# Kernel tuning notes

Measured on AMD Instinct MI355X. Metric: run time of the kernel, lower is better.

Reference implementation:

```python
import jax, jax.numpy as jnp
import numpy as np

B, S, D = 1, 4096, 1024
H, Dh = 16, 64
F = 4096  # mlp_factor * D
EPS = 1e-6


def _ln(x, scale, bias=None):
    m = jnp.mean(x, axis=-1, keepdims=True)
    v = jnp.var(x, axis=-1, keepdims=True)
    y = (x - m) * jax.lax.rsqrt(v + EPS) * scale
    return y + bias if bias is not None else y


def setup_inputs() -> dict:
    key = jax.random.key(0)
    ks = jax.random.split(key, 10)
    lecun = lambda k, shape, fan_in: (jax.random.normal(k, shape, jnp.float32) * (fan_in ** -0.5))
    inp = {
        "x": jax.random.normal(ks[0], (B, S, D), jnp.float32),
        # causal mask, broadcastable to [B, H, S, S]
        "mask": jnp.tril(jnp.ones((S, S), bool))[None, None],
        # PreNorm (TPNorm -> LayerNorm)
        "ln_scale": jnp.ones((D,), jnp.float32),
        "ln_bias": jnp.zeros((D,), jnp.float32),
        # MLP input projection
        "w_in": lecun(ks[1], (D, F), D),
        "b_in": jnp.zeros((F,), jnp.float32),
        # QKV projection
        "wq": lecun(ks[2], (D, H, Dh), D),
        "bq": jnp.zeros((H, Dh), jnp.float32),
        "wk": lecun(ks[3], (D, H, Dh), D),
        "bk": jnp.zeros((H, Dh), jnp.float32),
        "wv": lecun(ks[4], (D, H, Dh), D),
        "bv": jnp.zeros((H, Dh), jnp.float32),
        # qk-norm scales (normalize_qk=True)
        "qn_scale": jnp.ones((Dh,), jnp.float32),
        "kn_scale": jnp.ones((Dh,), jnp.float32),
        # MLP output projection
        "w_mo": lecun(ks[5], (F, D), F),
        "b_mo": jnp.zeros((D,), jnp.float32),
        # Attention output projection
        "w_ao": lecun(ks[6], (H * Dh, D), H * Dh),
        "b_ao": jnp.zeros((D,), jnp.float32),
    }
    return inp


def reference(x, mask, ln_scale, ln_bias, w_in, b_in, wq, bq, wk, bk, wv, bv,
              qn_scale, kn_scale, w_mo, b_mo, w_ao, b_ao):
    residual = x
    xn = _ln(x, ln_scale, ln_bias)

    # fused QKV + MLP-input projections (QKVMLPDenseParallel)
    h = jax.nn.gelu(jnp.einsum("bsd,df->bsf", xn, w_in) + b_in)  # [B,S,F]
    q = jnp.einsum("bsd,dhk->bshk", xn, wq) + bq  # [B,S,H,Dh]
    k = jnp.einsum("bsd,dhk->bshk", xn, wk) + bk
    v = jnp.einsum("bsd,dhk->bshk", xn, wv) + bv
    # normalize_qk: per-head LayerNorm (no bias) on q, k
    q = _ln(q, qn_scale)
    k = _ln(k, kn_scale)

    # dot-product attention
    scores = jnp.einsum("bqhd,bkhd->bhqk", q, k) / np.sqrt(Dh).astype(np.float32)
    scores = jnp.where(mask, scores, jnp.finfo(scores.dtype).min)
    attn = jax.nn.softmax(scores, axis=-1)
    o = jnp.einsum("bhqk,bkhd->bqhd", attn, v)  # [B,S,H,Dh]

    # fused attention-out + MLP-out projections (AttnMLPOutParallel)
    mlp_out = jnp.einsum("bsf,fd->bsd", h, w_mo) + b_mo
    attn_out = jnp.einsum("bse,ed->bsd", o.reshape(B, S, H * Dh), w_ao) + b_ao

    # dropout deterministic (train=False); residual add
    return residual + mlp_out + attn_out
```

## Files before the change

kernel.cpp:

```cpp
#include <hip/hip_runtime.h>
#include <hip/hip_fp16.h>

typedef _Float16 half8 __attribute__((ext_vector_type(8)));
typedef float floatx4 __attribute__((ext_vector_type(4)));

constexpr int kS = 4096;
constexpr int kD = 1024;
constexpr int kH = 16;
constexpr int kDh = 64;
constexpr int kF = 4096;
constexpr int kNQKV = kF + 3 * kD;
constexpr int kKOut = kF + kD;

__device__ __forceinline__ void async_ld16(const void* g, void* l) {
  __builtin_amdgcn_global_load_lds(
      (const __attribute__((address_space(1))) void*)g,
      (__attribute__((address_space(3))) void*)l, 16, 0, 0);
}

__global__ __launch_bounds__(256) void prep0_kernel(
    const float* __restrict__ w_in, const float* __restrict__ wq,
    const float* __restrict__ wk, const float* __restrict__ wv,
    const float* __restrict__ w_mo, const float* __restrict__ w_ao,
    _Float16* __restrict__ Wqkv, _Float16* __restrict__ Wout,
    const float* __restrict__ x, const float* __restrict__ ln_scale,
    const float* __restrict__ ln_bias, _Float16* __restrict__ xn) {
  __shared__ float t[32][33];
  __shared__ float red[8];
  int id = blockIdx.x;
  const int tid = threadIdx.x;

  if (id >= 12288) {
    const int row = id - 12288;
    const float* xr = x + (size_t)row * kD;
    float v[4];
    float s = 0.f, sq = 0.f;
#pragma unroll
    for (int i = 0; i < 4; ++i) {
      v[i] = xr[tid + 256 * i];
      s += v[i];
      sq += v[i] * v[i];
    }
    for (int off = 32; off; off >>= 1) {
      s += __shfl_xor(s, off);
      sq += __shfl_xor(sq, off);
    }
    const int wv2 = tid >> 6;
    if ((tid & 63) == 0) { red[wv2] = s; red[wv2 + 4] = sq; }
    __syncthreads();
    s = red[0] + red[1] + red[2] + red[3];
    sq = red[4] + red[5] + red[6] + red[7];
    const float mean = s * (1.0f / kD);
    const float var = sq * (1.0f / kD) - mean * mean;
    const float rstd = rsqrtf(var + 1e-6f);
#pragma unroll
    for (int i = 0; i < 4; ++i) {
      int d = tid + 256 * i;
      xn[(size_t)row * kD + d] = (_Float16)((v[i] - mean) * rstd * ln_scale[d] + ln_bias[d]);
    }
    return;
  }

  const float* src; _Float16* dst; int N, ldk, noff, koff, nt, kt;
  if (id < 4096)       { src = w_in; dst = Wqkv; N = kF; ldk = kD; noff = 0;        koff = 0;  nt = id & 127; kt = id >> 7; }
  else if (id < 5120)  { id -= 4096; src = wq;  dst = Wqkv; N = kD; ldk = kD; noff = kF;       koff = 0;  nt = id & 31; kt = id >> 5; }
  else if (id < 6144)  { id -= 5120; src = wk;  dst = Wqkv; N = kD; ldk = kD; noff = kF + kD;  koff = 0;  nt = id & 31; kt = id >> 5; }
  else if (id < 7168)  { id -= 6144; src = wv;  dst = Wqkv; N = kD; ldk = kD; noff = kF + 2*kD; koff = 0; nt = id & 31; kt = id >> 5; }
  else if (id < 11264) { id -= 7168; src = w_mo; dst = Wout; N = kD; ldk = kKOut; noff = 0;    koff = 0;  nt = id & 31; kt = id >> 5; }
  else                 { id -= 11264; src = w_ao; dst = Wout; N = kD; ldk = kKOut; noff = 0;   koff = kF; nt = id & 31; kt = id >> 5; }
  const int n0 = nt * 32, k0 = kt * 32;
#pragma unroll
  for (int i = 0; i < 4; ++i) {
    const int kl = (tid >> 5) + i * 8, nl = tid & 31;
    t[kl][nl] = src[(size_t)(k0 + kl) * N + n0 + nl];
  }
  __syncthreads();
#pragma unroll
  for (int i = 0; i < 4; ++i) {
    const int nl = (tid >> 5) + i * 8, kl = tid & 31;
    dst[(size_t)(noff + n0 + nl) * ldk + koff + k0 + kl] = (_Float16)t[kl][nl];
  }
}

__global__ __launch_bounds__(256) void htrans_kernel(
    const _Float16* __restrict__ src, _Float16* __restrict__ dst, int R, int C) {
  __shared__ _Float16 t[32][34];
  const int tid = threadIdx.x;
  const int c0 = blockIdx.x * 32, r0 = blockIdx.y * 32;
#pragma unroll
  for (int i = 0; i < 4; ++i) {
    const int rl = (tid >> 5) + i * 8, cl = tid & 31;
    t[rl][cl] = src[(size_t)(r0 + rl) * C + c0 + cl];
  }
  __syncthreads();
#pragma unroll
  for (int i = 0; i < 4; ++i) {
    const int cl = (tid >> 5) + i * 8, rl = tid & 31;
    dst[(size_t)(c0 + cl) * R + r0 + rl] = t[rl][cl];
  }
}

__device__ __forceinline__ float fast_gelu(float xv) {
  const float z = 0.7978845608028654f * (xv + 0.044715f * xv * xv * xv);
  const float u = exp2f(fminf(2.885390081777927f * z, 80.0f));
  return xv * u / (1.0f + u);
}

__global__ __launch_bounds__(256) void gemm_qkvin(
    const _Float16* __restrict__ A, const _Float16* __restrict__ Bp,
    const float* __restrict__ b_in, const float* __restrict__ bq,
    const float* __restrict__ bk, const float* __restrict__ bv,
    const float* __restrict__ qn_scale, const float* __restrict__ kn_scale,
    _Float16* __restrict__ ho, _Float16* __restrict__ q,
    _Float16* __restrict__ k, _Float16* __restrict__ v) {
  __shared__ alignas(16) _Float16 Ts[16 * 512];
  _Float16* As = Ts;
  _Float16* Bs = Ts + 8 * 512;

  const int tid = threadIdx.x;
  const int lane = tid & 63;
  const int wave = tid >> 6;
  const int wm = (wave >> 1) * 64;
  const int wn = (wave & 1) * 64;
  const int m0 = blockIdx.x * 128;
  const int n0 = blockIdx.y * 128;
  const int lrow = lane & 15;
  const int quad = lane >> 4;

  floatx4 acc[4][4] = {};

  for (int k0 = 0; k0 < kD; k0 += 32) {
    __syncthreads();
#pragma unroll
    for (int i = 0; i < 4; ++i) {
      const int chunk = wave * 4 + i;
      const int r = ((chunk & 7) << 4) + (lane >> 2);
      const int csrc = ((lane & 3) ^ ((r >> 1) & 3)) << 3;
      const _Float16* src = (chunk < 8)
          ? A + (size_t)(m0 + r) * kD + k0 + csrc
          : Bp + (size_t)(n0 + r) * kD + k0 + csrc;
      async_ld16(src, Ts + chunk * 512);
    }
    __syncthreads();

    half8 af[4], bf[4];
#pragma unroll
    for (int i = 0; i < 4; ++i) {
      const int ra = wm + i * 16 + lrow;
      const int rb = wn + i * 16 + lrow;
      af[i] = *reinterpret_cast<const half8*>(&As[ra * 32 + ((quad ^ ((ra >> 1) & 3)) << 3)]);
      bf[i] = *reinterpret_cast<const half8*>(&Bs[rb * 32 + ((quad ^ ((rb >> 1) & 3)) << 3)]);
    }
#pragma unroll
    for (int i = 0; i < 4; ++i)
#pragma unroll
      for (int j = 0; j < 4; ++j)
        acc[i][j] = __builtin_amdgcn_mfma_f32_16x16x32_f16(af[i], bf[j], acc[i][j], 0, 0, 0);
  }

  const int nblk = n0 + wn;
  if (nblk < kF) {
#pragma unroll
    for (int i = 0; i < 4; ++i) {
      const int gm = m0 + wm + i * 16 + quad * 4;
#pragma unroll
      for (int j = 0; j < 4; ++j) {
        const int gn = nblk + j * 16 + lrow;
        const float bn = b_in[gn];
#pragma unroll
        for (int r = 0; r < 4; ++r)
          ho[(size_t)(gm + r) * kKOut + gn] = (_Float16)fast_gelu(acc[i][j][r] + bn);
      }
    }
  } else if (nblk >= kF + 2 * kD) {
#pragma unroll
    for (int i = 0; i < 4; ++i) {
      const int gm = m0 + wm + i * 16 + quad * 4;
#pragma unroll
      for (int j = 0; j < 4; ++j) {
        const int gn = nblk + j * 16 + lrow;
        const float bn = bv[(gn - kF) & (kD - 1)];
#pragma unroll
        for (int r = 0; r < 4; ++r)
          v[(size_t)(gm + r) * kD + ((gn - kF) & (kD - 1))] = (_Float16)(acc[i][j][r] + bn);
      }
    }
  } else {
    const bool isq = nblk < kF + kD;
    const float* nsc = isq ? qn_scale : kn_scale;
    const float* nb = isq ? bq : bk;
    const float sm = isq ? 0.18033688f : 1.0f;
    _Float16* dst = isq ? q : k;
    const int col0 = (nblk - kF) & (kD - 1);
    float bj[4];
#pragma unroll
    for (int j = 0; j < 4; ++j) bj[j] = nb[col0 + j * 16 + lrow];
#pragma unroll
    for (int i = 0; i < 4; ++i) {
      const int gm = m0 + wm + i * 16 + quad * 4;
#pragma unroll
      for (int r = 0; r < 4; ++r) {
        float vals[4], s1 = 0.f, s2 = 0.f;
#pragma unroll
        for (int j = 0; j < 4; ++j) {
          const float vv = acc[i][j][r] + bj[j];
          vals[j] = vv; s1 += vv; s2 += vv * vv;
        }
#pragma unroll
        for (int off = 1; off <= 8; off <<= 1) {
          s1 += __shfl_xor(s1, off);
          s2 += __shfl_xor(s2, off);
        }
        const float mean = s1 * (1.0f / 64.0f);
        const float rstd = rsqrtf(s2 * (1.0f / 64.0f) - mean * mean + 1e-6f);
#pragma unroll
        for (int j = 0; j < 4; ++j) {
          const int d = j * 16 + lrow;
          dst[(size_t)(gm + r) * kD + col0 + d] =
              (_Float16)((vals[j] - mean) * rstd * nsc[d] * sm);
        }
      }
    }
  }
}

__global__ __launch_bounds__(256) void prep_kernel(
    const float* __restrict__ x, const float* __restrict__ b_mo,
    const float* __restrict__ b_ao, float* __restrict__ out,
    float* __restrict__ Oacc, float* __restrict__ Lacc) {
  const int i = blockIdx.x * 256 + threadIdx.x;
  if (i < kS * kD) {
    const int d = i & (kD - 1);
    out[i] = x[i] + b_mo[d] + b_ao[d];
    Oacc[i] = 0.f;
  } else if (i < kS * kD + kS * kH) {
    Lacc[i - kS * kD] = 0.f;
  }
}

__global__ __launch_bounds__(256) void gemm_out(
    const _Float16* __restrict__ A, const _Float16* __restrict__ Bp,
    float* __restrict__ out) {
  __shared__ alignas(16) _Float16 Ts[16 * 512];
  _Float16* As = Ts;
  _Float16* Bs = Ts + 8 * 512;

  const int tid = threadIdx.x;
  const int lane = tid & 63;
  const int wave = tid >> 6;
  const int wm = (wave >> 1) * 64;
  const int wn = (wave & 1) * 64;
  const int m0 = blockIdx.x * 128;
  const int n0 = blockIdx.y * 128;
  const int kbeg = blockIdx.z * (kKOut / 2);
  const int lrow = lane & 15;
  const int quad = lane >> 4;

  floatx4 acc[4][4] = {};

  for (int k0 = kbeg; k0 < kbeg + kKOut / 2; k0 += 32) {
    __syncthreads();
#pragma unroll
    for (int i = 0; i < 4; ++i) {
      const int chunk = wave * 4 + i;
      const int r = ((chunk & 7) << 4) + (lane >> 2);
      const int csrc = ((lane & 3) ^ ((r >> 1) & 3)) << 3;
      const _Float16* src = (chunk < 8)
          ? A + (size_t)(m0 + r) * kKOut + k0 + csrc
          : Bp + (size_t)(n0 + r) * kKOut + k0 + csrc;
      async_ld16(src, Ts + chunk * 512);
    }
    __syncthreads();

    half8 af[4], bf[4];
#pragma unroll
    for (int i = 0; i < 4; ++i) {
      const int ra = wm + i * 16 + lrow;
      const int rb = wn + i * 16 + lrow;
      af[i] = *reinterpret_cast<const half8*>(&As[ra * 32 + ((quad ^ ((ra >> 1) & 3)) << 3)]);
      bf[i] = *reinterpret_cast<const half8*>(&Bs[rb * 32 + ((quad ^ ((rb >> 1) & 3)) << 3)]);
    }
#pragma unroll
    for (int i = 0; i < 4; ++i)
#pragma unroll
      for (int j = 0; j < 4; ++j)
        acc[i][j] = __builtin_amdgcn_mfma_f32_16x16x32_f16(af[i], bf[j], acc[i][j], 0, 0, 0);
  }

#pragma unroll
  for (int i = 0; i < 4; ++i) {
    const int gm = m0 + wm + i * 16 + quad * 4;
#pragma unroll
    for (int j = 0; j < 4; ++j) {
      const int gn = n0 + wn + j * 16 + lrow;
#pragma unroll
      for (int r = 0; r < 4; ++r)
        atomicAdd(out + (size_t)(gm + r) * kD + gn, acc[i][j][r]);
    }
  }
}

__global__ __launch_bounds__(256) void fattn_kernel(
    const _Float16* __restrict__ Q, const _Float16* __restrict__ K,
    const _Float16* __restrict__ Vt, float* __restrict__ Oacc,
    float* __restrict__ Lacc) {
  __shared__ alignas(16) _Float16 Qs[64 * 64];
  __shared__ alignas(16) _Float16 Ks[64 * 64];
  __shared__ alignas(16) _Float16 Vs[64 * 64];
  __shared__ alignas(16) _Float16 Ps[64 * 72];

  const int tid = threadIdx.x;
  const int lane = tid & 63;
  const int wave = tid >> 6;
  const int lrow = lane & 15;
  const int quad = lane >> 4;
  const int h = blockIdx.y;
  const int pair = blockIdx.x;
  const int split = blockIdx.z;

  const int rs = lane >> 3;
  const int cs = lane & 7;
  constexpr float kOff = 11.5415603f;

  for (int pass = 0; pass < 2; ++pass) {
    const int qtile = pass ? (63 - pair) : pair;
    const int qbase = qtile * 64;

    __syncthreads();
#pragma unroll
    for (int i = 0; i < 2; ++i) {
      const int chunk = wave * 2 + i;
      const int r = chunk * 8 + rs;
      async_ld16(Q + (size_t)(qbase + r) * kD + h * kDh + ((cs ^ (r & 7)) << 3),
                 Qs + chunk * 512);
    }
    __syncthreads();

    half8 qf[2];
#pragma unroll
    for (int kt = 0; kt < 2; ++kt) {
      const int row = wave * 16 + lrow;
      qf[kt] = *reinterpret_cast<const half8*>(
          &Qs[row * 64 + (((kt * 4 + quad) ^ (row & 7)) << 3)]);
    }

    float lst[4] = {0.f, 0.f, 0.f, 0.f};
    floatx4 oacc[4] = {};
    const int qw = qbase + wave * 16;

    for (int t = split; t <= qtile; t += 2) {
      const int k0 = t * 64;
      __syncthreads();
#pragma unroll
      for (int i = 0; i < 4; ++i) {
        const int c2 = wave * 4 + i;
        if (c2 < 8) {
          const int r = c2 * 8 + rs;
          async_ld16(K + (size_t)(k0 + r) * kD + h * kDh + ((cs ^ (r & 7)) << 3),
                     Ks + c2 * 512);
        } else {
          const int c = c2 - 8;
          const int r = c * 8 + rs;
          async_ld16(Vt + (size_t)(h * kDh + r) * kS + k0 + ((cs ^ (r & 7)) << 3),
                     Vs + c * 512);
        }
      }
      __syncthreads();

      const bool diag = (t == qtile);

      floatx4 sacc[4] = {};
#pragma unroll
      for (int jt = 0; jt < 4; ++jt) {
        if (diag && jt > wave) continue;
#pragma unroll
        for (int kt = 0; kt < 2; ++kt) {
          const int rb = jt * 16 + lrow;
          half8 bfk = *reinterpret_cast<const half8*>(
              &Ks[rb * 64 + (((kt * 4 + quad) ^ (rb & 7)) << 3)]);
          sacc[jt] = __builtin_amdgcn_mfma_f32_16x16x32_f16(qf[kt], bfk, sacc[jt], 0, 0, 0);
        }
      }

      if (diag) {
#pragma unroll
        for (int jt = 0; jt < 4; ++jt) {
          const int kg = k0 + jt * 16 + lrow;
#pragma unroll
          for (int r = 0; r < 4; ++r)
            if (kg > qw + quad * 4 + r) sacc[jt][r] = -1e30f;
        }
      }

#pragma unroll
      for (int jt = 0; jt < 4; ++jt)
#pragma unroll
        for (int r = 0; r < 4; ++r) {
          const float p = exp2f(sacc[jt][r] - kOff);
          sacc[jt][r] = p;
          lst[r] += p;
        }

#pragma unroll
      for (int jt = 0; jt < 4; ++jt)
#pragma unroll
        for (int r = 0; r < 4; ++r)
          Ps[(wave * 16 + quad * 4 + r) * 72 + jt * 16 + lrow] = (_Float16)sacc[jt][r];

      const int ktmax = (diag && wave < 2) ? 1 : 2;
      for (int kt = 0; kt < ktmax; ++kt) {
        half8 pf = *reinterpret_cast<const half8*>(
            &Ps[(wave * 16 + lrow) * 72 + (kt * 4 + quad) * 8]);
#pragma unroll
        for (int jt = 0; jt < 4; ++jt) {
          const int rb = jt * 16 + lrow;
          half8 vf = *reinterpret_cast<const half8*>(
              &Vs[rb * 64 + (((kt * 4 + quad) ^ (rb & 7)) << 3)]);
          oacc[jt] = __builtin_amdgcn_mfma_f32_16x16x32_f16(pf, vf, oacc[jt], 0, 0, 0);
        }
      }
    }

#pragma unroll
    for (int r = 0; r < 4; ++r)
#pragma unroll
      for (int off = 8; off; off >>= 1) lst[r] += __shfl_xor(lst[r], off);
#pragma unroll
    for (int r = 0; r < 4; ++r) {
      const int qg = qw + quad * 4 + r;
      if (lrow == 0) atomicAdd(Lacc + qg * kH + h, lst[r]);
#pragma unroll
      for (int jt = 0; jt < 4; ++jt)
        atomicAdd(Oacc + ((size_t)qg * kH + h) * kDh + jt * 16 + lrow, oacc[jt][r]);
    }
  }
}

__global__ __launch_bounds__(256) void norm_kernel(
    const float* __restrict__ Oacc, const float* __restrict__ Lacc,
    _Float16* __restrict__ ho) {
  const int idx = blockIdx.x * 256 + threadIdx.x;
  const int q = idx >> 10, rem = idx & 1023;
  const float l = Lacc[(q << 4) + (rem >> 6)];
  ho[(size_t)q * kKOut + kF + rem] = (_Float16)(Oacc[idx] / l);
}

extern "C" void kernel_launch(void* const* d_in, const int* in_sizes, int n_in,
                              void* d_out, int out_size, void* d_ws, size_t ws_size,
                              hipStream_t stream) {
  const float* x        = (const float*)d_in[0];
  const float* ln_scale = (const float*)d_in[2];
  const float* ln_bias  = (const float*)d_in[3];
  const float* w_in     = (const float*)d_in[4];
  const float* b_in     = (const float*)d_in[5];
  const float* wq       = (const float*)d_in[6];
  const float* bq       = (const float*)d_in[7];
  const float* wk       = (const float*)d_in[8];
  const float* bk       = (const float*)d_in[9];
  const float* wv       = (const float*)d_in[10];
  const float* bv       = (const float*)d_in[11];
  const float* qn_scale = (const float*)d_in[12];
  const float* kn_scale = (const float*)d_in[13];
  const float* w_mo     = (const float*)d_in[14];
  const float* b_mo     = (const float*)d_in[15];
  const float* w_ao     = (const float*)d_in[16];
  const float* b_ao     = (const float*)d_in[17];
  float* out = (float*)d_out;

  char* ws = (char*)d_ws;
  size_t off = 0;
  auto alloc = [&](size_t bytes) { char* p = ws + off; off += bytes; return p; };
  char* zone = (char*)alloc((size_t)kS * kD * 2 + (size_t)kNQKV * kD * 2);
  _Float16* xn   = (_Float16*)zone;
  _Float16* Wqkv = (_Float16*)(zone + (size_t)kS * kD * 2);
  float* Oacc = (float*)zone;
  float* Lacc = (float*)(zone + (size_t)kS * kD * 4);
  _Float16* Wout = (_Float16*)alloc((size_t)kD * kKOut * 2);
  _Float16* ho   = (_Float16*)alloc((size_t)kS * kKOut * 2);
  _Float16* q_h  = (_Float16*)alloc((size_t)kS * kD * 2);
  _Float16* k_h  = (_Float16*)alloc((size_t)kS * kD * 2);
  _Float16* v_h  = (_Float16*)alloc((size_t)kS * kD * 2);
  _Float16* v_t  = (_Float16*)alloc((size_t)kS * kD * 2);

  prep0_kernel<<<12288 + 4096, 256, 0, stream>>>(
      w_in, wq, wk, wv, w_mo, w_ao, Wqkv, Wout, x, ln_scale, ln_bias, xn);

  gemm_qkvin<<<dim3(kS / 128, kNQKV / 128), 256, 0, stream>>>(
      xn, Wqkv, b_in, bq, bk, bv, qn_scale, kn_scale, ho, q_h, k_h, v_h);

  htrans_kernel<<<dim3(kD / 32, kS / 32), 256, 0, stream>>>(v_h, v_t, kS, kD);

  prep_kernel<<<(kS * kD + kS * kH + 255) / 256, 256, 0, stream>>>(
      x, b_mo, b_ao, out, Oacc, Lacc);

  fattn_kernel<<<dim3(32, kH, 2), 256, 0, stream>>>(q_h, k_h, v_t, Oacc, Lacc);

  norm_kernel<<<kS * kD / 256, 256, 0, stream>>>(Oacc, Lacc, ho);

  gemm_out<<<dim3(kS / 128, kD / 128, 2), 256, 0, stream>>>(ho, Wout, out);
}
```

Measured before the change: 460.8 us.

## Double-buffer LDS tiles in QKV-input and output GEMMs to overlap loads

Both fp16 MFMA GEMM kernels move from a single shared-memory tile to two ping-pong buffers. The next k-slice is prefetched with async global-to-LDS loads while MFMAs run on the current slice, and one waitcnt plus barrier per iteration replaces the previous pair of syncthreads. The aim is to hide global load latency behind compute. In exchange LDS use doubles to 32KB per block, which may reduce occupancy, and the raw s_barrier with no lgkmcnt wait relies on the compiler ordering the LDS reads before the next overwrite.

```diff
diff --git a/kernel.cpp b/kernel.cpp
--- a/kernel.cpp
+++ b/kernel.cpp
@@ -113,9 +113,7 @@
     const float* __restrict__ qn_scale, const float* __restrict__ kn_scale,
     _Float16* __restrict__ ho, _Float16* __restrict__ q,
     _Float16* __restrict__ k, _Float16* __restrict__ v) {
-  __shared__ alignas(16) _Float16 Ts[16 * 512];
-  _Float16* As = Ts;
-  _Float16* Bs = Ts + 8 * 512;
+  __shared__ alignas(16) _Float16 Ts[2][16 * 512];
 
   const int tid = threadIdx.x;
   const int lane = tid & 63;
@@ -129,8 +127,7 @@
 
   floatx4 acc[4][4] = {};
 
-  for (int k0 = 0; k0 < kD; k0 += 32) {
-    __syncthreads();
+  auto stage = [&](int buf, int k0) {
 #pragma unroll
     for (int i = 0; i < 4; ++i) {
       const int chunk = wave * 4 + i;
@@ -139,10 +136,20 @@
       const _Float16* src = (chunk < 8)
           ? A + (size_t)(m0 + r) * kD + k0 + csrc
           : Bp + (size_t)(n0 + r) * kD + k0 + csrc;
-      async_ld16(src, Ts + chunk * 512);
-    }
-    __syncthreads();
-
+      async_ld16(src, &Ts[buf][chunk * 512]);
+    }
+  };
+
+  stage(0, 0);
+  asm volatile("s_waitcnt vmcnt(0)" ::: "memory");
+  __builtin_amdgcn_s_barrier();
+
+  int cur = 0;
+  for (int k0 = 0; k0 < kD; k0 += 32) {
+    if (k0 + 32 < kD) stage(cur ^ 1, k0 + 32);
+
+    const _Float16* As = Ts[cur];
+    const _Float16* Bs = Ts[cur] + 8 * 512;
     half8 af[4], bf[4];
 #pragma unroll
     for (int i = 0; i < 4; ++i) {
@@ -156,6 +163,10 @@
 #pragma unroll
       for (int j = 0; j < 4; ++j)
         acc[i][j] = __builtin_amdgcn_mfma_f32_16x16x32_f16(af[i], bf[j], acc[i][j], 0, 0, 0);
+
+    asm volatile("s_waitcnt vmcnt(0)" ::: "memory");
+    __builtin_amdgcn_s_barrier();
+    cur ^= 1;
   }
 
   const int nblk = n0 + wn;
@@ -241,9 +252,7 @@
 __global__ __launch_bounds__(256) void gemm_out(
     const _Float16* __restrict__ A, const _Float16* __restrict__ Bp,
     float* __restrict__ out) {
-  __shared__ alignas(16) _Float16 Ts[16 * 512];
-  _Float16* As = Ts;
-  _Float16* Bs = Ts + 8 * 512;
+  __shared__ alignas(16) _Float16 Ts[2][16 * 512];
 
   const int tid = threadIdx.x;
   const int lane = tid & 63;
@@ -253,13 +262,13 @@
   const int m0 = blockIdx.x * 128;
   const int n0 = blockIdx.y * 128;
   const int kbeg = blockIdx.z * (kKOut / 2);
+  const int kend = kbeg + kKOut / 2;
   const int lrow = lane & 15;
   const int quad = lane >> 4;
 
   floatx4 acc[4][4] = {};
 
-  for (int k0 = kbeg; k0 < kbeg + kKOut / 2; k0 += 32) {
-    __syncthreads();
+  auto stage = [&](int buf, int k0) {
 #pragma unroll
     for (int i = 0; i < 4; ++i) {
       const int chunk = wave * 4 + i;
@@ -268,10 +277,20 @@
       const _Float16* src = (chunk < 8)
           ? A + (size_t)(m0 + r) * kKOut + k0 + csrc
           : Bp + (size_t)(n0 + r) * kKOut + k0 + csrc;
-      async_ld16(src, Ts + chunk * 512);
-    }
-    __syncthreads();
-
+      async_ld16(src, &Ts[buf][chunk * 512]);
+    }
+  };
+
+  stage(0, kbeg);
+  asm volatile("s_waitcnt vmcnt(0)" ::: "memory");
+  __builtin_amdgcn_s_barrier();
+
+  int cur = 0;
+  for (int k0 = kbeg; k0 < kend; k0 += 32) {
+    if (k0 + 32 < kend) stage(cur ^ 1, k0 + 32);
+
+    const _Float16* As = Ts[cur];
+    const _Float16* Bs = Ts[cur] + 8 * 512;
     half8 af[4], bf[4];
 #pragma unroll
     for (int i = 0; i < 4; ++i) {
@@ -285,6 +304,10 @@
 #pragma unroll
       for (int j = 0; j < 4; ++j)
         acc[i][j] = __builtin_amdgcn_mfma_f32_16x16x32_f16(af[i], bf[j], acc[i][j], 0, 0, 0);
+
+    asm volatile("s_waitcnt vmcnt(0)" ::: "memory");
+    __builtin_amdgcn_s_barrier();
+    cur ^= 1;
   }
 
 #pragma unroll
```

New measurement: 451.5 us. -2.0%, faster.
